# Performance work log

Hardware: AMD Instinct MI355X
Metric: run time of the kernel (lower is better)

## Reference

```python
import jax, jax.numpy as jnp
import numpy as np

# Structural hyperparams (mirror init_kwargs)
G, Q, C, D = 2, 8, 1024, 8          # groups, quantizers/group, codebook_size, codebook_dim
DIMS = 1024                          # residual_fsq.dim
DPG = DIMS // G                      # dim per group (project_out output)
B, L = 4, 4096                       # batch, frame length
UP_K, UP_S = 4, 2                    # upsample ConvTranspose1d kernel/stride
HEAD_K, HEAD_OUT = 7, 512            # head Conv1d kernel / out channels


def setup_inputs() -> dict:
    key = jax.random.key(0)
    ks = jax.random.split(key, 8)
    indices = jax.random.randint(ks[0], (B, G * Q, L), 0, C, dtype=jnp.int64)
    codebooks = jax.random.normal(ks[1], (G, Q, C, D), jnp.float32)
    scales = jax.random.uniform(ks[2], (G, Q, D), jnp.float32, 0.5, 2.0)
    W_out = jax.random.normal(ks[3], (G, D, DPG), jnp.float32) * (1.0 / np.sqrt(D))
    b_out = jnp.zeros((G, DPG), jnp.float32)
    W_up = jax.random.normal(ks[4], (DIMS, DIMS, UP_K), jnp.float32) * 0.02   # IOH layout
    b_up = jnp.zeros((DIMS,), jnp.float32)
    W_head = jax.random.normal(ks[5], (HEAD_OUT, DIMS, HEAD_K), jnp.float32) * 0.02  # OIH
    b_head = jnp.zeros((HEAD_OUT,), jnp.float32)
    return dict(indices=indices, codebooks=codebooks, scales=scales,
                W_out=W_out, b_out=b_out, W_up=W_up, b_up=b_up,
                W_head=W_head, b_head=b_head)


def reference(indices, codebooks, scales, W_out, b_out, W_up, b_up, W_head, b_head):
    b, gq, l = indices.shape
    g, q = codebooks.shape[0], codebooks.shape[1]
    # [B, G*Q, L] -> [G, B, L, Q]  (matches view + permute in forward)
    idx = indices.reshape(b, g, q, l).transpose(1, 0, 3, 2)
    mask = idx == -1                              # dropout-padded codes
    idx0 = jnp.where(mask, 0, idx)
    # gather codes per (group, quantizer): codebooks[g, q, idx0[g,b,l,q]] -> [G,B,L,Q,D]
    g_ix = jnp.arange(g)[:, None, None, None]
    q_ix = jnp.arange(q)[None, None, None, :]
    codes = codebooks[g_ix, q_ix, idx0]
    # mask, scale, sum over quantizers (residual sum)
    codes = jnp.where(mask[..., None], 0.0, codes) * scales[:, None, None, :, :]
    summed = codes.sum(axis=3)                    # [G,B,L,D]
    # per-group project_out: Linear(D -> DPG)
    z = jnp.einsum('gbld,gde->gble', summed, W_out) + b_out[:, None, None, :]
    # concat groups along feature dim -> [B, L, DIMS], then NCH for convs
    z_q = z.transpose(1, 2, 0, 3).reshape(b, l, g * z.shape[-1])
    zc = z_q.transpose(0, 2, 1)                   # [B, DIMS, L]
    # upsample: ConvTranspose1d(DIMS->DIMS, k=4, stride=2) -> [B, DIMS, 2L]
    zu = jax.lax.conv_transpose(zc, W_up, strides=(UP_S,), padding='SAME',
                                dimension_numbers=('NCH', 'IOH', 'NCH'))
    zu = zu + b_up[None, :, None]
    # head: Conv1d(DIMS -> HEAD_OUT, k=7, same padding)
    x = jax.lax.conv_general_dilated(zu, W_head, window_strides=(1,), padding='SAME',
                                     dimension_numbers=('NCH', 'OIH', 'NCH'))
    x = x + b_head[None, :, None]
    return x
```

## Files before the change

### kernel.cpp

```cpp
#include <hip/hip_runtime.h>
#include <hip/hip_bf16.h>

typedef __attribute__((ext_vector_type(8))) short bf16x8;
typedef __attribute__((ext_vector_type(4))) float f32x4;

#define GQ 16
#define L_IN 4096
#define T_UP 8192
#define CB 1024
#define ZROWS 4098
#define UROWS 8198

__device__ __forceinline__ void gload16(const void* g, void* l) {
    __builtin_amdgcn_global_load_lds((const __attribute__((address_space(1))) void*)g,
                                     (__attribute__((address_space(3))) void*)l, 16, 0, 0);
}

__global__ __launch_bounds__(256) void zero_pads(__hip_bfloat16* __restrict__ zp,
                                                 __hip_bfloat16* __restrict__ zup) {
    int idx = blockIdx.x * 256 + threadIdx.x;
    if (idx < 8192) {
        int b = idx >> 11, rs = (idx >> 10) & 1, c = idx & 1023;
        size_t row = (size_t)b * ZROWS + (rs ? (ZROWS - 1) : 0);
        zp[row * 1024 + c] = __float2bfloat16(0.f);
    } else if (idx < 8192 + 24576) {
        int rem = idx - 8192;
        int b = rem / 6144, r2 = rem % 6144;
        int r6 = r2 >> 10, c = r2 & 1023;
        size_t row = (size_t)b * UROWS + (r6 < 3 ? r6 : (UROWS - 6 + r6));
        zup[row * 1024 + c] = __float2bfloat16(0.f);
    }
}

__global__ __launch_bounds__(256) void repack_up(const float* __restrict__ Wup,
                                                 __hip_bfloat16* __restrict__ Wr) {
    int idx = blockIdx.x * 256 + threadIdx.x;
    int kk = idx >> 20;
    int co = (idx >> 10) & 1023;
    int ci = idx & 1023;
    Wr[idx] = __float2bfloat16(Wup[((ci << 10) + co) * 4 + kk]);
}

__global__ __launch_bounds__(256) void repack_head(const float* __restrict__ Wh,
                                                   __hip_bfloat16* __restrict__ Wr) {
    int idx = blockIdx.x * 256 + threadIdx.x;
    int kk = idx >> 19;
    int rem = idx & ((1 << 19) - 1);
    int o = rem >> 10;
    int ci = rem & 1023;
    Wr[idx] = __float2bfloat16(Wh[(o * 1024 + ci) * 7 + kk]);
}

__global__ __launch_bounds__(256) void dequant_project(
    const int* __restrict__ indices, const float* __restrict__ codebooks,
    const float* __restrict__ scales, const float* __restrict__ Wout,
    const float* __restrict__ bout, __hip_bfloat16* __restrict__ z)
{
    __shared__ float w_lds[8192];
    __shared__ float b_lds[1024];
    __shared__ float part[128];
    __shared__ float summed[16];
    int tid = threadIdx.x;
    for (int k = tid; k < 8192; k += 256) w_lds[k] = Wout[k];
    for (int k = tid; k < 1024; k += 256) b_lds[k] = bout[k];
    int p0 = blockIdx.x * 16;
    int b  = p0 >> 12;
    int l0 = p0 & 4095;
    __syncthreads();
    for (int i = 0; i < 16; ++i) {
        int l = l0 + i;
        if (tid < 128) {
            int gq = tid >> 3;
            int d  = tid & 7;
            int idx = indices[(b * GQ + gq) * L_IN + l];
            float v = 0.f;
            if (idx >= 0) {
                int ic = (idx < CB) ? idx : 0;
                v = codebooks[(gq * CB + ic) * 8 + d] * scales[gq * 8 + d];
            }
            part[tid] = v;
        }
        __syncthreads();
        if (tid < 16) {
            int g = tid >> 3, d = tid & 7;
            float s = 0.f;
            for (int q = 0; q < 8; ++q) s += part[(g * 8 + q) * 8 + d];
            summed[tid] = s;
        }
        __syncthreads();
        #pragma unroll
        for (int j = 0; j < 4; ++j) {
            int c = tid + j * 256;
            int g = c >> 9;
            float acc = b_lds[c];
            #pragma unroll
            for (int d = 0; d < 8; ++d)
                acc += summed[g * 8 + d] * w_lds[(g * 8 + d) * 512 + (c & 511)];
            z[((size_t)b * ZROWS + l + 1) * 1024 + c] = __float2bfloat16(acc);
        }
        __syncthreads();
    }
}

__global__ __launch_bounds__(256, 2) void conv_up_mfma(
    const __hip_bfloat16* __restrict__ zp, const __hip_bfloat16* __restrict__ Wr,
    const float* __restrict__ bup, __hip_bfloat16* __restrict__ zup)
{
    __shared__ __hip_bfloat16 Als[2][128][64];
    __shared__ __hip_bfloat16 Bls[2][128][64];
    const int tid = threadIdx.x;
    const int lane = tid & 63;
    const int w = tid >> 6;
    const int wm = w >> 1, wn = w & 1;
    const int l15 = lane & 15, kq = lane >> 4;
    const int m0  = blockIdx.x * 128;
    const int co0 = blockIdx.y * 128;
    const int b = blockIdx.z >> 1, P = blockIdx.z & 1;

    const __hip_bfloat16* zb = zp + ((size_t)b * ZROWS + m0 + P) * 1024;
    const __hip_bfloat16* wb = Wr + ((size_t)P * 1024 + co0) * 1024;

    auto stage = [&](int buf, int s) {
        int j = s & 1, ci0 = (s >> 1) << 6;
        const __hip_bfloat16* sa = zb + (size_t)j * 1024 + ci0;
        const __hip_bfloat16* sb = wb + (size_t)j * 2048 * 1024 + ci0;
        #pragma unroll
        for (int it = 0; it < 4; ++it) {
            int chunk = it * 256 + tid;
            int row = chunk >> 3, cs = chunk & 7;
            int cq = cs ^ (row & 7);
            gload16(sa + (size_t)row * 1024 + cq * 8,
                    (char*)&Als[buf][0][0] + ((it * 256 + (w << 6)) << 4));
            gload16(sb + (size_t)row * 1024 + cq * 8,
                    (char*)&Bls[buf][0][0] + ((it * 256 + (w << 6)) << 4));
        }
    };

    const f32x4 zero4 = {0.f, 0.f, 0.f, 0.f};
    f32x4 acc[4][4];
    #pragma unroll
    for (int r = 0; r < 4; ++r)
        #pragma unroll
        for (int c = 0; c < 4; ++c) acc[r][c] = zero4;

    stage(0, 0);
    __syncthreads();
    int cur = 0;
    for (int s = 0; s < 32; ++s) {
        if (s + 1 < 32) stage(cur ^ 1, s + 1);
        bf16x8 af[2][4], bfr[2][4];
        #pragma unroll
        for (int sl = 0; sl < 2; ++sl) {
            #pragma unroll
            for (int r = 0; r < 4; ++r) {
                int row = (wm << 6) + r * 16 + l15;
                int pc = (sl * 4 + kq) ^ (row & 7);
                af[sl][r] = *(const bf16x8*)&Als[cur][row][pc * 8];
            }
            #pragma unroll
            for (int c = 0; c < 4; ++c) {
                int row = (wn << 6) + c * 16 + l15;
                int pc = (sl * 4 + kq) ^ (row & 7);
                bfr[sl][c] = *(const bf16x8*)&Bls[cur][row][pc * 8];
            }
        }
        __builtin_amdgcn_s_setprio(1);
        #pragma unroll
        for (int sl = 0; sl < 2; ++sl)
            #pragma unroll
            for (int r = 0; r < 4; ++r)
                #pragma unroll
                for (int c = 0; c < 4; ++c)
                    acc[r][c] = __builtin_amdgcn_mfma_f32_16x16x32_bf16(
                        af[sl][r], bfr[sl][c], acc[r][c], 0, 0, 0);
        __builtin_amdgcn_s_setprio(0);
        __syncthreads();
        cur ^= 1;
    }

    const int mb  = m0 + (wm << 6) + (kq << 2);
    const int cob = co0 + (wn << 6) + l15;
    #pragma unroll
    for (int c = 0; c < 4; ++c) {
        float bias = bup[cob + c * 16];
        #pragma unroll
        for (int r = 0; r < 4; ++r)
            #pragma unroll
            for (int e = 0; e < 4; ++e) {
                int m = mb + r * 16 + e;
                zup[((size_t)b * UROWS + 3 + P + 2 * m) * 1024 + cob + c * 16] =
                    __float2bfloat16(acc[r][c][e] + bias);
            }
    }
}

__global__ __launch_bounds__(256, 2) void conv_head_mfma(
    const __hip_bfloat16* __restrict__ zup, const __hip_bfloat16* __restrict__ Wr,
    const float* __restrict__ bh, float* __restrict__ out)
{
    __shared__ __hip_bfloat16 Als[2][128][64];
    __shared__ __hip_bfloat16 Bls[2][128][64];
    const int tid = threadIdx.x;
    const int lane = tid & 63;
    const int w = tid >> 6;
    const int wm = w >> 1, wn = w & 1;
    const int l15 = lane & 15, kq = lane >> 4;
    const int t0 = blockIdx.x * 128;
    const int o0 = blockIdx.y * 128;
    const int b  = blockIdx.z;

    const __hip_bfloat16* wb = Wr + (size_t)o0 * 1024;
    const __hip_bfloat16* zb = zup + ((size_t)b * UROWS + t0) * 1024;

    auto stage = [&](int buf, int kk, int ci0) {
        const __hip_bfloat16* sa = wb + (size_t)kk * 512 * 1024 + ci0;
        const __hip_bfloat16* sb = zb + (size_t)kk * 1024 + ci0;
        #pragma unroll
        for (int it = 0; it < 4; ++it) {
            int chunk = it * 256 + tid;
            int row = chunk >> 3, cs = chunk & 7;
            int cq = cs ^ (row & 7);
            gload16(sa + (size_t)row * 1024 + cq * 8,
                    (char*)&Als[buf][0][0] + ((it * 256 + (w << 6)) << 4));
            gload16(sb + (size_t)row * 1024 + cq * 8,
                    (char*)&Bls[buf][0][0] + ((it * 256 + (w << 6)) << 4));
        }
    };

    const f32x4 zero4 = {0.f, 0.f, 0.f, 0.f};
    f32x4 acc[4][4];
    #pragma unroll
    for (int r = 0; r < 4; ++r)
        #pragma unroll
        for (int c = 0; c < 4; ++c) acc[r][c] = zero4;

    int nk = 0, nc = 0;
    stage(0, nk, nc);
    if (++nk == 7) { nk = 0; nc += 64; }
    __syncthreads();
    int cur = 0;
    for (int s = 0; s < 112; ++s) {
        if (s + 1 < 112) {
            stage(cur ^ 1, nk, nc);
            if (++nk == 7) { nk = 0; nc += 64; }
        }
        bf16x8 af[2][4], bfr[2][4];
        #pragma unroll
        for (int sl = 0; sl < 2; ++sl) {
            #pragma unroll
            for (int r = 0; r < 4; ++r) {
                int row = (wm << 6) + r * 16 + l15;
                int pc = (sl * 4 + kq) ^ (row & 7);
                af[sl][r] = *(const bf16x8*)&Als[cur][row][pc * 8];
            }
            #pragma unroll
            for (int c = 0; c < 4; ++c) {
                int row = (wn << 6) + c * 16 + l15;
                int pc = (sl * 4 + kq) ^ (row & 7);
                bfr[sl][c] = *(const bf16x8*)&Bls[cur][row][pc * 8];
            }
        }
        __builtin_amdgcn_s_setprio(1);
        #pragma unroll
        for (int sl = 0; sl < 2; ++sl)
            #pragma unroll
            for (int r = 0; r < 4; ++r)
                #pragma unroll
                for (int c = 0; c < 4; ++c)
                    acc[r][c] = __builtin_amdgcn_mfma_f32_16x16x32_bf16(
                        af[sl][r], bfr[sl][c], acc[r][c], 0, 0, 0);
        __builtin_amdgcn_s_setprio(0);
        __syncthreads();
        cur ^= 1;
    }

    const int ob = o0 + (wm << 6) + (kq << 2);
    const int tb = t0 + (wn << 6) + l15;
    #pragma unroll
    for (int r = 0; r < 4; ++r)
        #pragma unroll
        for (int e = 0; e < 4; ++e) {
            int o = ob + r * 16 + e;
            float bias = bh[o];
            #pragma unroll
            for (int c = 0; c < 4; ++c)
                out[((size_t)b * 512 + o) * T_UP + tb + c * 16] = acc[r][c][e] + bias;
        }
}

extern "C" void kernel_launch(void* const* d_in, const int* in_sizes, int n_in,
                              void* d_out, int out_size, void* d_ws, size_t ws_size,
                              hipStream_t stream) {
    const int*   indices   = (const int*)d_in[0];
    const float* codebooks = (const float*)d_in[1];
    const float* scales    = (const float*)d_in[2];
    const float* Wout      = (const float*)d_in[3];
    const float* bout      = (const float*)d_in[4];
    const float* Wup       = (const float*)d_in[5];
    const float* bup       = (const float*)d_in[6];
    const float* Wh        = (const float*)d_in[7];
    const float* bh        = (const float*)d_in[8];
    float* out = (float*)d_out;

    __hip_bfloat16* zp    = (__hip_bfloat16*)d_ws;
    __hip_bfloat16* zup   = zp + (size_t)4 * ZROWS * 1024;
    __hip_bfloat16* wr_up = zup + (size_t)4 * UROWS * 1024;
    __hip_bfloat16* wr_h  = wr_up + (size_t)4 * 1024 * 1024;

    zero_pads  <<<dim3(128),   dim3(256), 0, stream>>>(zp, zup);
    repack_up  <<<dim3(16384), dim3(256), 0, stream>>>(Wup, wr_up);
    repack_head<<<dim3(14336), dim3(256), 0, stream>>>(Wh, wr_h);
    dequant_project<<<dim3(1024), dim3(256), 0, stream>>>(indices, codebooks, scales,
                                                          Wout, bout, zp);
    conv_up_mfma  <<<dim3(32, 8, 8), dim3(256), 0, stream>>>(zp, wr_up, bup, zup);
    conv_head_mfma<<<dim3(64, 4, 4), dim3(256), 0, stream>>>(zup, wr_h, bh, out);
}
```

Baseline: 514.0 us.

## Use 256x256 tiles with 8-wave interleaved load/MFMA pipeline in conv GEMMs

Both the transposed-conv and head-conv MFMA kernels move from 128x128 tiles with 4 waves to 256x256 tiles with 8 waves. Global-to-LDS staging is split into quarter-tile parts interleaved with MFMA quadrants, using explicit vmcnt/lgkmcnt waits and raw barriers. The aim is to raise arithmetic intensity per loaded byte and to hide memory latency behind matrix math. The cost is fewer blocks (the head grid fills each CU only once), heavy LDS use that limits occupancy, and a fragile hand-counted wait schedule.

New measurement: 466.6 us. -9.2%, faster.

```diff
diff --git a/kernel.cpp b/kernel.cpp
--- a/kernel.cpp
+++ b/kernel.cpp
@@ -15,6 +15,24 @@
     __builtin_amdgcn_global_load_lds((const __attribute__((address_space(1))) void*)g,
                                      (__attribute__((address_space(3))) void*)l, 16, 0, 0);
 }
+
+#define SB()  __builtin_amdgcn_s_barrier()
+#define LGKM() do { asm volatile("s_waitcnt lgkmcnt(0)" ::: "memory"); \
+                    __builtin_amdgcn_sched_barrier(0); } while (0)
+#define VMW(n) do { __builtin_amdgcn_sched_barrier(0); \
+                    asm volatile("s_waitcnt vmcnt(" #n ")" ::: "memory"); \
+                    __builtin_amdgcn_sched_barrier(0); } while (0)
+
+#define MM(MH, NH) do {                                                          \
+    __builtin_amdgcn_s_setprio(1);                                               \
+    _Pragma("unroll") for (int j_ = 0; j_ < 4; ++j_)                             \
+      _Pragma("unroll") for (int n_ = 0; n_ < 2; ++n_)                           \
+        _Pragma("unroll") for (int s_ = 0; s_ < 2; ++s_)                         \
+          acc[(MH)*4 + j_][(NH)*2 + n_] = __builtin_amdgcn_mfma_f32_16x16x32_bf16( \
+              af[j_][s_], bq[(NH)*2 + n_][s_], acc[(MH)*4 + j_][(NH)*2 + n_],    \
+              0, 0, 0);                                                          \
+    __builtin_amdgcn_s_setprio(0);                                               \
+} while (0)
 
 __global__ __launch_bounds__(256) void zero_pads(__hip_bfloat16* __restrict__ zp,
                                                  __hip_bfloat16* __restrict__ zup) {
@@ -102,189 +120,237 @@
     }
 }
 
-__global__ __launch_bounds__(256, 2) void conv_up_mfma(
+
+__global__ __launch_bounds__(512, 2) void conv_up_mfma(
     const __hip_bfloat16* __restrict__ zp, const __hip_bfloat16* __restrict__ Wr,
     const float* __restrict__ bup, __hip_bfloat16* __restrict__ zup)
 {
-    __shared__ __hip_bfloat16 Als[2][128][64];
-    __shared__ __hip_bfloat16 Bls[2][128][64];
+    __shared__ __hip_bfloat16 Als[2][256][64];
+    __shared__ __hip_bfloat16 Bls[2][256][64];
     const int tid = threadIdx.x;
     const int lane = tid & 63;
     const int w = tid >> 6;
-    const int wm = w >> 1, wn = w & 1;
+    const int wm = w >> 2, wn = w & 3;
     const int l15 = lane & 15, kq = lane >> 4;
-    const int m0  = blockIdx.x * 128;
-    const int co0 = blockIdx.y * 128;
+    const int m0  = blockIdx.x * 256;
+    const int co0 = blockIdx.y * 256;
     const int b = blockIdx.z >> 1, P = blockIdx.z & 1;
-
-    const __hip_bfloat16* zb = zp + ((size_t)b * ZROWS + m0 + P) * 1024;
-    const __hip_bfloat16* wb = Wr + ((size_t)P * 1024 + co0) * 1024;
-
-    auto stage = [&](int buf, int s) {
-        int j = s & 1, ci0 = (s >> 1) << 6;
-        const __hip_bfloat16* sa = zb + (size_t)j * 1024 + ci0;
-        const __hip_bfloat16* sb = wb + (size_t)j * 2048 * 1024 + ci0;
-        #pragma unroll
-        for (int it = 0; it < 4; ++it) {
-            int chunk = it * 256 + tid;
+    const int NT = 32, NIT = 16;
+
+    const __hip_bfloat16* abase = zp + ((size_t)b * ZROWS + m0 + P) * 1024;
+    const __hip_bfloat16* bbase = Wr + ((size_t)P * 1024 + co0) * 1024;
+
+    auto stage = [&](int kt, int part) {
+        if (kt >= NT) return;
+        const int buf = kt & 1;
+        const int j = kt >> 4, ci0 = (kt & 15) << 6;
+        const int rb = (part & 1) << 7;
+        const __hip_bfloat16* src;
+        __hip_bfloat16* dst;
+        if (part < 2) { src = abase + ((size_t)j + rb) * 1024 + ci0;
+                        dst = &Als[buf][rb][0]; }
+        else          { src = bbase + ((size_t)j * 2048 + rb) * 1024 + ci0;
+                        dst = &Bls[buf][rb][0]; }
+        #pragma unroll
+        for (int it = 0; it < 2; ++it) {
+            int chunk = it * 512 + tid;
             int row = chunk >> 3, cs = chunk & 7;
             int cq = cs ^ (row & 7);
-            gload16(sa + (size_t)row * 1024 + cq * 8,
-                    (char*)&Als[buf][0][0] + ((it * 256 + (w << 6)) << 4));
-            gload16(sb + (size_t)row * 1024 + cq * 8,
-                    (char*)&Bls[buf][0][0] + ((it * 256 + (w << 6)) << 4));
-        }
-    };
-
-    const f32x4 zero4 = {0.f, 0.f, 0.f, 0.f};
-    f32x4 acc[4][4];
-    #pragma unroll
-    for (int r = 0; r < 4; ++r)
-        #pragma unroll
-        for (int c = 0; c < 4; ++c) acc[r][c] = zero4;
-
-    stage(0, 0);
-    __syncthreads();
-    int cur = 0;
-    for (int s = 0; s < 32; ++s) {
-        if (s + 1 < 32) stage(cur ^ 1, s + 1);
-        bf16x8 af[2][4], bfr[2][4];
-        #pragma unroll
-        for (int sl = 0; sl < 2; ++sl) {
-            #pragma unroll
-            for (int r = 0; r < 4; ++r) {
-                int row = (wm << 6) + r * 16 + l15;
-                int pc = (sl * 4 + kq) ^ (row & 7);
-                af[sl][r] = *(const bf16x8*)&Als[cur][row][pc * 8];
-            }
-            #pragma unroll
-            for (int c = 0; c < 4; ++c) {
-                int row = (wn << 6) + c * 16 + l15;
-                int pc = (sl * 4 + kq) ^ (row & 7);
-                bfr[sl][c] = *(const bf16x8*)&Bls[cur][row][pc * 8];
-            }
-        }
-        __builtin_amdgcn_s_setprio(1);
-        #pragma unroll
-        for (int sl = 0; sl < 2; ++sl)
-            #pragma unroll
-            for (int r = 0; r < 4; ++r)
-                #pragma unroll
-                for (int c = 0; c < 4; ++c)
-                    acc[r][c] = __builtin_amdgcn_mfma_f32_16x16x32_bf16(
-                        af[sl][r], bfr[sl][c], acc[r][c], 0, 0, 0);
-        __builtin_amdgcn_s_setprio(0);
-        __syncthreads();
-        cur ^= 1;
+            gload16(src + (size_t)row * 1024 + cq * 8,
+                    (char*)dst + ((it * 512 + (w << 6)) << 4));
+        }
+    };
+
+    f32x4 acc[8][4];
+    const f32x4 z4 = {0.f, 0.f, 0.f, 0.f};
+    #pragma unroll
+    for (int i = 0; i < 8; ++i)
+        #pragma unroll
+        for (int j = 0; j < 4; ++j) acc[i][j] = z4;
+
+    bf16x8 af[4][2], bq[4][2];
+
+    auto rdA = [&](int buf, int mh) {
+        #pragma unroll
+        for (int j = 0; j < 4; ++j)
+            #pragma unroll
+            for (int sl = 0; sl < 2; ++sl) {
+                int row = (wm << 7) + (mh << 6) + j * 16 + l15;
+                int ch = (sl * 4 + kq) ^ (row & 7);
+                af[j][sl] = *(const bf16x8*)&Als[buf][row][ch * 8];
+            }
+    };
+    auto rdB = [&](int buf) {
+        #pragma unroll
+        for (int nf = 0; nf < 4; ++nf)
+            #pragma unroll
+            for (int sl = 0; sl < 2; ++sl) {
+                int row = (wn << 6) + nf * 16 + l15;
+                int ch = (sl * 4 + kq) ^ (row & 7);
+                bq[nf][sl] = *(const bf16x8*)&Bls[buf][row][ch * 8];
+            }
+    };
+
+    stage(0, 2); stage(0, 3); stage(0, 0); stage(0, 1);
+    stage(1, 2); stage(1, 3); stage(1, 0);
+    VMW(6);
+    SB();
+
+    for (int it = 0; it < NIT; ++it) {
+        const bool lastit = (it == NIT - 1);
+        rdA(0, 0); rdB(0);
+        stage(2 * it + 1, 1);
+        SB(); LGKM(); MM(0, 0); SB();
+        stage(2 * it + 2, 2);
+        SB(); MM(0, 1); SB();
+        rdA(0, 1);
+        stage(2 * it + 2, 3);
+        SB(); LGKM(); MM(1, 1); SB();
+        stage(2 * it + 2, 0);
+        if (lastit) { VMW(0); } else { VMW(6); }
+        SB(); MM(1, 0); SB();
+        rdA(1, 0); rdB(1);
+        stage(2 * it + 2, 1);
+        SB(); LGKM(); MM(0, 0); SB();
+        stage(2 * it + 3, 2);
+        SB(); MM(0, 1); SB();
+        rdA(1, 1);
+        stage(2 * it + 3, 3);
+        SB(); LGKM(); MM(1, 1); SB();
+        stage(2 * it + 3, 0);
+        if (!lastit) { VMW(6); }
+        SB(); MM(1, 0); SB();
     }
 
-    const int mb  = m0 + (wm << 6) + (kq << 2);
+    float bias[4];
+    #pragma unroll
+    for (int nf = 0; nf < 4; ++nf) bias[nf] = bup[co0 + (wn << 6) + nf * 16 + l15];
+    const int mbase = m0 + (wm << 7) + (kq << 2);
     const int cob = co0 + (wn << 6) + l15;
     #pragma unroll
-    for (int c = 0; c < 4; ++c) {
-        float bias = bup[cob + c * 16];
-        #pragma unroll
-        for (int r = 0; r < 4; ++r)
-            #pragma unroll
-            for (int e = 0; e < 4; ++e) {
-                int m = mb + r * 16 + e;
-                zup[((size_t)b * UROWS + 3 + P + 2 * m) * 1024 + cob + c * 16] =
-                    __float2bfloat16(acc[r][c][e] + bias);
-            }
-    }
-}
-
-__global__ __launch_bounds__(256, 2) void conv_head_mfma(
+    for (int mf = 0; mf < 8; ++mf)
+        #pragma unroll
+        for (int e = 0; e < 4; ++e) {
+            int m = mbase + mf * 16 + e;
+            size_t rowoff = ((size_t)b * UROWS + 3 + P + 2 * m) * 1024;
+            #pragma unroll
+            for (int nf = 0; nf < 4; ++nf)
+                zup[rowoff + cob + nf * 16] = __float2bfloat16(acc[mf][nf][e] + bias[nf]);
+        }
+}
+
+__global__ __launch_bounds__(512, 2) void conv_head_mfma(
     const __hip_bfloat16* __restrict__ zup, const __hip_bfloat16* __restrict__ Wr,
     const float* __restrict__ bh, float* __restrict__ out)
 {
-    __shared__ __hip_bfloat16 Als[2][128][64];
-    __shared__ __hip_bfloat16 Bls[2][128][64];
+    __shared__ __hip_bfloat16 Als[2][256][64];
+    __shared__ __hip_bfloat16 Bls[2][256][64];
     const int tid = threadIdx.x;
     const int lane = tid & 63;
     const int w = tid >> 6;
-    const int wm = w >> 1, wn = w & 1;
+    const int wm = w >> 2, wn = w & 3;
     const int l15 = lane & 15, kq = lane >> 4;
-    const int t0 = blockIdx.x * 128;
-    const int o0 = blockIdx.y * 128;
+    const int t0 = blockIdx.x * 256;
+    const int o0 = blockIdx.y * 256;
     const int b  = blockIdx.z;
-
-    const __hip_bfloat16* wb = Wr + (size_t)o0 * 1024;
-    const __hip_bfloat16* zb = zup + ((size_t)b * UROWS + t0) * 1024;
-
-    auto stage = [&](int buf, int kk, int ci0) {
-        const __hip_bfloat16* sa = wb + (size_t)kk * 512 * 1024 + ci0;
-        const __hip_bfloat16* sb = zb + (size_t)kk * 1024 + ci0;
-        #pragma unroll
-        for (int it = 0; it < 4; ++it) {
-            int chunk = it * 256 + tid;
+    const int NT = 112, NIT = 56;
+
+    const __hip_bfloat16* bbase = zup + ((size_t)b * UROWS + t0) * 1024;
+
+    auto stage = [&](int kt, int part) {
+        if (kt >= NT) return;
+        const int buf = kt & 1;
+        const int kk = kt >> 4, ci0 = (kt & 15) << 6;
+        const int rb = (part & 1) << 7;
+        const __hip_bfloat16* src;
+        __hip_bfloat16* dst;
+        if (part < 2) { src = Wr + ((size_t)(kk * 512 + o0 + rb)) * 1024 + ci0;
+                        dst = &Als[buf][rb][0]; }
+        else          { src = bbase + ((size_t)(kk + rb)) * 1024 + ci0;
+                        dst = &Bls[buf][rb][0]; }
+        #pragma unroll
+        for (int it = 0; it < 2; ++it) {
+            int chunk = it * 512 + tid;
             int row = chunk >> 3, cs = chunk & 7;
             int cq = cs ^ (row & 7);
-            gload16(sa + (size_t)row * 1024 + cq * 8,
-                    (char*)&Als[buf][0][0] + ((it * 256 + (w << 6)) << 4));
-            gload16(sb + (size_t)row * 1024 + cq * 8,
-                    (char*)&Bls[buf][0][0] + ((it * 256 + (w << 6)) << 4));
-        }
-    };
-
-    const f32x4 zero4 = {0.f, 0.f, 0.f, 0.f};
-    f32x4 acc[4][4];
-    #pragma unroll
-    for (int r = 0; r < 4; ++r)
-        #pragma unroll
-        for (int c = 0; c < 4; ++c) acc[r][c] = zero4;
-
-    int nk = 0, nc = 0;
-    stage(0, nk, nc);
-    if (++nk == 7) { nk = 0; nc += 64; }
-    __syncthreads();
-    int cur = 0;
-    for (int s = 0; s < 112; ++s) {
-        if (s + 1 < 112) {
-            stage(cur ^ 1, nk, nc);
-            if (++nk == 7) { nk = 0; nc += 64; }
-        }
-        bf16x8 af[2][4], bfr[2][4];
-        #pragma unroll
-        for (int sl = 0; sl < 2; ++sl) {
-            #pragma unroll
-            for (int r = 0; r < 4; ++r) {
-                int row = (wm << 6) + r * 16 + l15;
-                int pc = (sl * 4 + kq) ^ (row & 7);
-                af[sl][r] = *(const bf16x8*)&Als[cur][row][pc * 8];
-            }
-            #pragma unroll
-            for (int c = 0; c < 4; ++c) {
-                int row = (wn << 6) + c * 16 + l15;
-                int pc = (sl * 4 + kq) ^ (row & 7);
-                bfr[sl][c] = *(const bf16x8*)&Bls[cur][row][pc * 8];
-            }
-        }
-        __builtin_amdgcn_s_setprio(1);
-        #pragma unroll
-        for (int sl = 0; sl < 2; ++sl)
-            #pragma unroll
-            for (int r = 0; r < 4; ++r)
-                #pragma unroll
-                for (int c = 0; c < 4; ++c)
-                    acc[r][c] = __builtin_amdgcn_mfma_f32_16x16x32_bf16(
-                        af[sl][r], bfr[sl][c], acc[r][c], 0, 0, 0);
-        __builtin_amdgcn_s_setprio(0);
-        __syncthreads();
-        cur ^= 1;
+            gload16(src + (size_t)row * 1024 + cq * 8,
+                    (char*)dst + ((it * 512 + (w << 6)) << 4));
+        }
+    };
+
+    f32x4 acc[8][4];
+    const f32x4 z4 = {0.f, 0.f, 0.f, 0.f};
+    #pragma unroll
+    for (int i = 0; i < 8; ++i)
+        #pragma unroll
+        for (int j = 0; j < 4; ++j) acc[i][j] = z4;
+
+    bf16x8 af[4][2], bq[4][2];
+
+    auto rdA = [&](int buf, int mh) {
+        #pragma unroll
+        for (int j = 0; j < 4; ++j)
+            #pragma unroll
+            for (int sl = 0; sl < 2; ++sl) {
+                int row = (wm << 7) + (mh << 6) + j * 16 + l15;
+                int ch = (sl * 4 + kq) ^ (row & 7);
+                af[j][sl] = *(const bf16x8*)&Als[buf][row][ch * 8];
+            }
+    };
+    auto rdB = [&](int buf) {
+        #pragma unroll
+        for (int nf = 0; nf < 4; ++nf)
+            #pragma unroll
+            for (int sl = 0; sl < 2; ++sl) {
+                int row = (wn << 6) + nf * 16 + l15;
+                int ch = (sl * 4 + kq) ^ (row & 7);
+                bq[nf][sl] = *(const bf16x8*)&Bls[buf][row][ch * 8];
+            }
+    };
+
+    stage(0, 2); stage(0, 3); stage(0, 0); stage(0, 1);
+    stage(1, 2); stage(1, 3); stage(1, 0);
+    VMW(6);
+    SB();
+
+    for (int it = 0; it < NIT; ++it) {
+        const bool lastit = (it == NIT - 1);
+        rdA(0, 0); rdB(0);
+        stage(2 * it + 1, 1);
+        SB(); LGKM(); MM(0, 0); SB();
+        stage(2 * it + 2, 2);
+        SB(); MM(0, 1); SB();
+        rdA(0, 1);
+        stage(2 * it + 2, 3);
+        SB(); LGKM(); MM(1, 1); SB();
+        stage(2 * it + 2, 0);
+        if (lastit) { VMW(0); } else { VMW(6); }
+        SB(); MM(1, 0); SB();
+        rdA(1, 0); rdB(1);
+        stage(2 * it + 2, 1);
+        SB(); LGKM(); MM(0, 0); SB();
+        stage(2 * it + 3, 2);
+        SB(); MM(0, 1); SB();
+        rdA(1, 1);
+        stage(2 * it + 3, 3);
+        SB(); LGKM(); MM(1, 1); SB();
+        stage(2 * it + 3, 0);
+        if (!lastit) { VMW(6); }
+        SB(); MM(1, 0); SB();
     }
 
-    const int ob = o0 + (wm << 6) + (kq << 2);
-    const int tb = t0 + (wn << 6) + l15;
-    #pragma unroll
-    for (int r = 0; r < 4; ++r)
+    const int obase = o0 + (wm << 7) + (kq << 2);
+    const int tbase = t0 + (wn << 6) + l15;
+    #pragma unroll
+    for (int mf = 0; mf < 8; ++mf)
         #pragma unroll
         for (int e = 0; e < 4; ++e) {
-            int o = ob + r * 16 + e;
+            int o = obase + mf * 16 + e;
             float bias = bh[o];
-            #pragma unroll
-            for (int c = 0; c < 4; ++c)
-                out[((size_t)b * 512 + o) * T_UP + tb + c * 16] = acc[r][c][e] + bias;
+            size_t rowoff = ((size_t)b * 512 + o) * T_UP + tbase;
+            #pragma unroll
+            for (int nf = 0; nf < 4; ++nf)
+                out[rowoff + nf * 16] = acc[mf][nf][e] + bias;
         }
 }
 
@@ -312,6 +378,6 @@
     repack_head<<<dim3(14336), dim3(256), 0, stream>>>(Wh, wr_h);
     dequant_project<<<dim3(1024), dim3(256), 0, stream>>>(indices, codebooks, scales,
                                                           Wout, bout, zp);
-    conv_up_mfma  <<<dim3(32, 8, 8), dim3(256), 0, stream>>>(zp, wr_up, bup, zup);
-    conv_head_mfma<<<dim3(64, 4, 4), dim3(256), 0, stream>>>(zup, wr_h, bh, out);
-}
+    conv_up_mfma  <<<dim3(16, 4, 8), dim3(512), 0, stream>>>(zp, wr_up, bup, zup);
+    conv_head_mfma<<<dim3(32, 2, 4), dim3(512), 0, stream>>>(zup, wr_h, bh, out);
+}
```
